# Kernel optimization log

Measured on AMD Instinct MI355X. Metric: run time of the kernel, lower is better.

## Reference

```python
import jax, jax.numpy as jnp
import numpy as np

N = 100000   # num nodes
E = 1600000  # num edges (avg degree 16)
D = 64       # feature dim (in_size == out_size, proj unused in forward_dglsp)
EPS = 1e-12  # F.normalize eps


def setup_inputs() -> dict:
    key = jax.random.key(0)
    k1, k2, k3 = jax.random.split(key, 3)
    H = jax.random.normal(k1, (N, D), dtype=jnp.float32)
    row = jnp.sort(jax.random.randint(k2, (E,), 0, N, dtype=jnp.int64))  # dst (CSR-like)
    col = jax.random.randint(k3, (E,), 0, N, dtype=jnp.int64)            # src
    return {"H": H, "row": row, "col": col, "num_nodes": N}


def reference(H, row, col, num_nodes):
    # F.normalize(H, p=2, dim=1): divide by max(||h||, eps)
    norm = jnp.sqrt(jnp.sum(H * H, axis=1, keepdims=True))
    Hn = H / jnp.maximum(norm, EPS)

    # bsddmm(A, Hn, Hn.T): cosine-sim score per edge (r, c) = Hn[r] . Hn[c]
    scores = jnp.sum(Hn[row] * Hn[col], axis=1)  # [E]

    # edge softmax per destination row (dglsp softmax along last dim)
    m = jax.ops.segment_max(scores, row, num_segments=num_nodes)  # [N]
    e = jnp.exp(scores - m[row])
    s = jax.ops.segment_sum(e, row, num_segments=num_nodes)       # [N]
    attn = e / s[row]                                             # [E]

    # bspmm(attn, H): out[r] = sum over edges (r,c) attn * H[c]
    out = jax.ops.segment_sum(attn[:, None] * H[col], row, num_segments=num_nodes)
    return out  # [N, D]
```

## Files before the change

kernel.cpp:

```cpp
#include <hip/hip_runtime.h>
#include <math.h>

#define D 64
#define EPS 1e-12f
#define LOG2E 1.4426950408889634f

typedef _Float16 half4_t __attribute__((ext_vector_type(4)));

__device__ __forceinline__ float dpp_sum16(float s) {
    int x;
    x = __builtin_amdgcn_update_dpp(__float_as_int(s), __float_as_int(s),
                                    0x124, 0xf, 0xf, false);
    s += __int_as_float(x);
    x = __builtin_amdgcn_update_dpp(__float_as_int(s), __float_as_int(s),
                                    0x128, 0xf, 0xf, false);
    s += __int_as_float(x);
    x = __builtin_amdgcn_update_dpp(__float_as_int(s), __float_as_int(s),
                                    0xB1, 0xf, 0xf, false);
    s += __int_as_float(x);
    x = __builtin_amdgcn_update_dpp(__float_as_int(s), __float_as_int(s),
                                    0x4E, 0xf, 0xf, false);
    s += __int_as_float(x);
    return s;
}

__global__ void prep_kernel(const float4* __restrict__ H4,
                            float* __restrict__ inv_norm,
                            float* __restrict__ in_log,
                            half4_t* __restrict__ Hh,
                            const int* __restrict__ row,
                            int* __restrict__ row_ptr, int N, int E,
                            int do_conv) {
    int t = blockIdx.x * blockDim.x + threadIdx.x;
    if (t < N * 16) {
        int r = t >> 4, sub = t & 15;
        float4 v = H4[(size_t)r * 16 + sub];
        if (do_conv) {
            half4_t h;
            h[0] = (_Float16)v.x; h[1] = (_Float16)v.y;
            h[2] = (_Float16)v.z; h[3] = (_Float16)v.w;
            Hh[(size_t)r * 16 + sub] = h;
        }
        float ss = v.x * v.x + v.y * v.y + v.z * v.z + v.w * v.w;
        ss += __shfl_xor(ss, 1, 64);
        ss += __shfl_xor(ss, 2, 64);
        ss += __shfl_xor(ss, 4, 64);
        ss += __shfl_xor(ss, 8, 64);
        if (sub == 0) {
            float inv = 1.0f / fmaxf(sqrtf(ss), EPS);
            inv_norm[r] = inv;
            if (do_conv) in_log[r] = inv * LOG2E;
        }
    }
    if (t < E) {
        int cur  = row[t];
        int prev = (t == 0) ? -1 : row[t - 1];
        for (int r = prev + 1; r <= cur; ++r) row_ptr[r] = t;
        if (t == E - 1) {
            for (int r = cur + 1; r <= N; ++r) row_ptr[r] = E;
        }
    }
}

template <bool FP16>
__global__ __launch_bounds__(256) void agnn_kernel(
    const float* __restrict__ H,
    const half4_t* __restrict__ Hh,
    const float* __restrict__ inv_norm,
    const float* __restrict__ invg,
    const int* __restrict__ row_ptr,
    const int* __restrict__ col,
    float* __restrict__ out, int N) {
    int wid  = (blockIdx.x * blockDim.x + threadIdx.x) >> 6;
    int lane = threadIdx.x & 63;
    if (wid >= N) return;
    int g   = lane >> 4;
    int sub = lane & 15;

    int start = row_ptr[wid];
    int end   = row_ptr[wid + 1];

    if (start >= end) {
        if (g == 0) {
            float4 z = {0.0f, 0.0f, 0.0f, 0.0f};
            ((float4*)out)[(size_t)wid * 16 + sub] = z;
        }
        return;
    }

    const float4* H4 = (const float4*)H;
    const char* Hb   = (const char*)(FP16 ? (const void*)Hh : (const void*)H);
    const char* Ib   = (const char*)invg;
    const char* Cb   = (const char*)col;
    unsigned subo    = (unsigned)sub << (FP16 ? 3 : 4);

    auto ld_row = [&](int c) -> float4 {
        if constexpr (FP16) {
            half4_t h = *(const half4_t*)(Hb + (((unsigned)c << 7) + subo));
            float4 f;
            f.x = (float)h[0]; f.y = (float)h[1];
            f.z = (float)h[2]; f.w = (float)h[3];
            return f;
        } else {
            return *(const float4*)(Hb + (((unsigned)c << 8) + subo));
        }
    };
    auto ld_in  = [&](int c) -> float { return *(const float*)(Ib + ((unsigned)c << 2)); };
    auto ld_col = [&](int i) -> int   { return *(const int*)(Cb + ((unsigned)i << 2)); };
    auto edge_p = [&](float s, float in) -> float {
        if constexpr (FP16) return exp2f(s * in);
        else                return __expf(s * in);
    };

    float4 hr = H4[(size_t)wid * 16 + sub];
    float inr = inv_norm[wid];
    hr.x *= inr; hr.y *= inr; hr.z *= inr; hr.w *= inr;

    float  l = 0.0f;
    float4 acc = {0.0f, 0.0f, 0.0f, 0.0f};

    int e  = start + g;
    int cl = end - 1;

    int c0 = ld_col(min(e, cl));
    int c1 = ld_col(min(e + 4, cl));
    float  in0 = ld_in(c0),  in1 = ld_in(c1);
    float4 h0  = ld_row(c0), h1  = ld_row(c1);

    while (e + 4 < end) {
        int n0 = ld_col(min(e + 8,  cl));
        int n1 = ld_col(min(e + 12, cl));
        float  nin0 = ld_in(n0),  nin1 = ld_in(n1);
        float4 nh0  = ld_row(n0), nh1  = ld_row(n1);

        float s0 = hr.x * h0.x + hr.y * h0.y + hr.z * h0.z + hr.w * h0.w;
        float s1 = hr.x * h1.x + hr.y * h1.y + hr.z * h1.z + hr.w * h1.w;
        s0 = dpp_sum16(s0);
        s1 = dpp_sum16(s1);

        float p0 = edge_p(s0, in0);
        float p1 = edge_p(s1, in1);
        l += p0 + p1;
        acc.x += p0 * h0.x + p1 * h1.x;
        acc.y += p0 * h0.y + p1 * h1.y;
        acc.z += p0 * h0.z + p1 * h1.z;
        acc.w += p0 * h0.w + p1 * h1.w;

        h0 = nh0; h1 = nh1; in0 = nin0; in1 = nin1;
        e += 8;
    }

    if (e < end) {
        float s = hr.x * h0.x + hr.y * h0.y + hr.z * h0.z + hr.w * h0.w;
        s = dpp_sum16(s);
        float p = edge_p(s, in0);
        l += p;
        acc.x += p * h0.x;
        acc.y += p * h0.y;
        acc.z += p * h0.z;
        acc.w += p * h0.w;
    }

    #pragma unroll
    for (int off = 16; off <= 32; off <<= 1) {
        l     += __shfl_xor(l, off, 64);
        acc.x += __shfl_xor(acc.x, off, 64);
        acc.y += __shfl_xor(acc.y, off, 64);
        acc.z += __shfl_xor(acc.z, off, 64);
        acc.w += __shfl_xor(acc.w, off, 64);
    }

    if (g == 0) {
        float invl = 1.0f / l;
        float4 o;
        o.x = acc.x * invl; o.y = acc.y * invl;
        o.z = acc.z * invl; o.w = acc.w * invl;
        ((float4*)out)[(size_t)wid * 16 + sub] = o;
    }
}

extern "C" void kernel_launch(void* const* d_in, const int* in_sizes, int n_in,
                              void* d_out, int out_size, void* d_ws, size_t ws_size,
                              hipStream_t stream) {
    const float* H   = (const float*)d_in[0];
    const int*   row = (const int*)d_in[1];
    const int*   col = (const int*)d_in[2];
    float*       out = (float*)d_out;

    int N = in_sizes[0] / D;
    int E = in_sizes[1];

    size_t hh_bytes = (size_t)N * 16 * sizeof(half4_t);
    size_t need     = hh_bytes + (size_t)N * 8 + (size_t)(N + 1) * 4;
    bool   use_fp16 = ws_size >= need;

    half4_t* Hh;
    float*   inv_norm;
    float*   in_log;
    int*     row_ptr;
    if (use_fp16) {
        Hh       = (half4_t*)d_ws;
        inv_norm = (float*)((char*)d_ws + hh_bytes);
        in_log   = inv_norm + N;
        row_ptr  = (int*)(in_log + N);
    } else {
        Hh       = (half4_t*)d_ws;
        inv_norm = (float*)d_ws;
        in_log   = inv_norm;
        row_ptr  = (int*)(inv_norm + N);
    }

    int prep_threads = (N * 16 > E) ? N * 16 : E;
    prep_kernel<<<(prep_threads + 255) / 256, 256, 0, stream>>>(
        (const float4*)H, inv_norm, in_log, Hh, row, row_ptr, N, E,
        use_fp16 ? 1 : 0);

    if (use_fp16) {
        agnn_kernel<true><<<(N + 3) / 4, 256, 0, stream>>>(
            H, Hh, inv_norm, in_log, row_ptr, col, out, N);
    } else {
        agnn_kernel<false><<<(N + 3) / 4, 256, 0, stream>>>(
            H, Hh, inv_norm, inv_norm, row_ptr, col, out, N);
    }
}
```

Measured before the change: 140.3 us.

## Precompute per-edge offset/invnorm pairs and batch eight gathers per iteration

Result: slower. 180.3 us (+28.5%).

```diff
diff --git a/kernel.cpp b/kernel.cpp
--- a/kernel.cpp
+++ b/kernel.cpp
@@ -24,52 +24,58 @@
     return s;
 }
 
-__global__ void prep_kernel(const float4* __restrict__ H4,
-                            float* __restrict__ inv_norm,
-                            float* __restrict__ in_log,
-                            half4_t* __restrict__ Hh,
-                            const int* __restrict__ row,
-                            int* __restrict__ row_ptr, int N, int E,
-                            int do_conv) {
+__global__ void prep1_kernel(const float4* __restrict__ H4,
+                             float* __restrict__ inv_norm,
+                             half4_t* __restrict__ Hh, int N, int do_conv) {
     int t = blockIdx.x * blockDim.x + threadIdx.x;
-    if (t < N * 16) {
-        int r = t >> 4, sub = t & 15;
-        float4 v = H4[(size_t)r * 16 + sub];
-        if (do_conv) {
-            half4_t h;
-            h[0] = (_Float16)v.x; h[1] = (_Float16)v.y;
-            h[2] = (_Float16)v.z; h[3] = (_Float16)v.w;
-            Hh[(size_t)r * 16 + sub] = h;
-        }
-        float ss = v.x * v.x + v.y * v.y + v.z * v.z + v.w * v.w;
-        ss += __shfl_xor(ss, 1, 64);
-        ss += __shfl_xor(ss, 2, 64);
-        ss += __shfl_xor(ss, 4, 64);
-        ss += __shfl_xor(ss, 8, 64);
-        if (sub == 0) {
-            float inv = 1.0f / fmaxf(sqrtf(ss), EPS);
-            inv_norm[r] = inv;
-            if (do_conv) in_log[r] = inv * LOG2E;
-        }
-    }
-    if (t < E) {
-        int cur  = row[t];
-        int prev = (t == 0) ? -1 : row[t - 1];
-        for (int r = prev + 1; r <= cur; ++r) row_ptr[r] = t;
-        if (t == E - 1) {
-            for (int r = cur + 1; r <= N; ++r) row_ptr[r] = E;
-        }
-    }
-}
-
-template <bool FP16>
-__global__ __launch_bounds__(256) void agnn_kernel(
+    if (t >= N * 16) return;
+    int r = t >> 4, sub = t & 15;
+    float4 v = H4[(size_t)r * 16 + sub];
+    if (do_conv) {
+        half4_t h;
+        h[0] = (_Float16)v.x; h[1] = (_Float16)v.y;
+        h[2] = (_Float16)v.z; h[3] = (_Float16)v.w;
+        Hh[(size_t)r * 16 + sub] = h;
+    }
+    float ss = v.x * v.x + v.y * v.y + v.z * v.z + v.w * v.w;
+    ss += __shfl_xor(ss, 1, 64);
+    ss += __shfl_xor(ss, 2, 64);
+    ss += __shfl_xor(ss, 4, 64);
+    ss += __shfl_xor(ss, 8, 64);
+    if (sub == 0) inv_norm[r] = 1.0f / fmaxf(sqrtf(ss), EPS);
+}
+
+__global__ void prep2_kernel(const int* __restrict__ row,
+                             const int* __restrict__ col,
+                             const float* __restrict__ inv_norm,
+                             int* __restrict__ row_ptr,
+                             uint2* __restrict__ pairs,
+                             int N, int E, int mode) {
+    int e = blockIdx.x * blockDim.x + threadIdx.x;
+    if (e >= E) return;
+    int cur  = row[e];
+    int prev = (e == 0) ? -1 : row[e - 1];
+    for (int r = prev + 1; r <= cur; ++r) row_ptr[r] = e;
+    if (e == E - 1) {
+        for (int r = cur + 1; r <= N; ++r) row_ptr[r] = E;
+    }
+    if (mode) {
+        int c = col[e];
+        uint2 pq;
+        pq.x = (unsigned)c << (mode == 1 ? 7 : 8);
+        pq.y = __float_as_uint(inv_norm[c] * LOG2E);
+        pairs[e] = pq;
+    }
+}
+
+template <bool FP16, bool PAIRS>
+__global__ __launch_bounds__(256, 8) void agnn_kernel(
     const float* __restrict__ H,
     const half4_t* __restrict__ Hh,
     const float* __restrict__ inv_norm,
-    const float* __restrict__ invg,
+    const uint2* __restrict__ pairs,
+    const int* __restrict__ col,
     const int* __restrict__ row_ptr,
-    const int* __restrict__ col,
     float* __restrict__ out, int N) {
     int wid  = (blockIdx.x * blockDim.x + threadIdx.x) >> 6;
     int lane = threadIdx.x & 63;
@@ -88,86 +94,77 @@
         return;
     }
 
-    const float4* H4 = (const float4*)H;
-    const char* Hb   = (const char*)(FP16 ? (const void*)Hh : (const void*)H);
-    const char* Ib   = (const char*)invg;
-    const char* Cb   = (const char*)col;
-    unsigned subo    = (unsigned)sub << (FP16 ? 3 : 4);
-
-    auto ld_row = [&](int c) -> float4 {
-        if constexpr (FP16) {
-            half4_t h = *(const half4_t*)(Hb + (((unsigned)c << 7) + subo));
-            float4 f;
-            f.x = (float)h[0]; f.y = (float)h[1];
-            f.z = (float)h[2]; f.w = (float)h[3];
-            return f;
-        } else {
-            return *(const float4*)(Hb + (((unsigned)c << 8) + subo));
-        }
-    };
-    auto ld_in  = [&](int c) -> float { return *(const float*)(Ib + ((unsigned)c << 2)); };
-    auto ld_col = [&](int i) -> int   { return *(const int*)(Cb + ((unsigned)i << 2)); };
-    auto edge_p = [&](float s, float in) -> float {
-        if constexpr (FP16) return exp2f(s * in);
-        else                return __expf(s * in);
-    };
-
-    float4 hr = H4[(size_t)wid * 16 + sub];
+    const char* Hb = FP16 ? (const char*)Hh : (const char*)H;
+    unsigned subo  = (unsigned)sub << (FP16 ? 3 : 4);
+
+    float4 hr = ((const float4*)H)[(size_t)wid * 16 + sub];
     float inr = inv_norm[wid];
     hr.x *= inr; hr.y *= inr; hr.z *= inr; hr.w *= inr;
 
     float  l = 0.0f;
     float4 acc = {0.0f, 0.0f, 0.0f, 0.0f};
-
-    int e  = start + g;
     int cl = end - 1;
 
-    int c0 = ld_col(min(e, cl));
-    int c1 = ld_col(min(e + 4, cl));
-    float  in0 = ld_in(c0),  in1 = ld_in(c1);
-    float4 h0  = ld_row(c0), h1  = ld_row(c1);
-
-    while (e + 4 < end) {
-        int n0 = ld_col(min(e + 8,  cl));
-        int n1 = ld_col(min(e + 12, cl));
-        float  nin0 = ld_in(n0),  nin1 = ld_in(n1);
-        float4 nh0  = ld_row(n0), nh1  = ld_row(n1);
-
-        float s0 = hr.x * h0.x + hr.y * h0.y + hr.z * h0.z + hr.w * h0.w;
-        float s1 = hr.x * h1.x + hr.y * h1.y + hr.z * h1.z + hr.w * h1.w;
-        s0 = dpp_sum16(s0);
-        s1 = dpp_sum16(s1);
-
-        float p0 = edge_p(s0, in0);
-        float p1 = edge_p(s1, in1);
-        l += p0 + p1;
-        acc.x += p0 * h0.x + p1 * h1.x;
-        acc.y += p0 * h0.y + p1 * h1.y;
-        acc.z += p0 * h0.z + p1 * h1.z;
-        acc.w += p0 * h0.w + p1 * h1.w;
-
-        h0 = nh0; h1 = nh1; in0 = nin0; in1 = nin1;
-        e += 8;
-    }
-
-    if (e < end) {
-        float s = hr.x * h0.x + hr.y * h0.y + hr.z * h0.z + hr.w * h0.w;
-        s = dpp_sum16(s);
-        float p = edge_p(s, in0);
-        l += p;
-        acc.x += p * h0.x;
-        acc.y += p * h0.y;
-        acc.z += p * h0.z;
-        acc.w += p * h0.w;
+    for (int base = start; base < end; base += 32) {
+        unsigned off[8];
+        float    inl[8];
+        #pragma unroll
+        for (int s = 0; s < 8; ++s) {
+            int ee = min(base + g + 4 * s, cl);
+            if constexpr (PAIRS) {
+                uint2 pq = pairs[ee];
+                off[s] = pq.x;
+                inl[s] = __uint_as_float(pq.y);
+            } else {
+                int c  = col[ee];
+                off[s] = (unsigned)c << (FP16 ? 7 : 8);
+                inl[s] = inv_norm[c] * LOG2E;
+            }
+        }
+        if constexpr (FP16) {
+            half4_t hh[8];
+            #pragma unroll
+            for (int s = 0; s < 8; ++s)
+                hh[s] = *(const half4_t*)(Hb + off[s] + subo);
+            #pragma unroll
+            for (int s = 0; s < 8; ++s) {
+                float4 h;
+                h.x = (float)hh[s][0]; h.y = (float)hh[s][1];
+                h.z = (float)hh[s][2]; h.w = (float)hh[s][3];
+                float sd = hr.x * h.x + hr.y * h.y + hr.z * h.z + hr.w * h.w;
+                sd = dpp_sum16(sd);
+                float p = exp2f(sd * inl[s]);
+                p = (base + g + 4 * s < end) ? p : 0.0f;
+                l += p;
+                acc.x += p * h.x; acc.y += p * h.y;
+                acc.z += p * h.z; acc.w += p * h.w;
+            }
+        } else {
+            float4 h[8];
+            #pragma unroll
+            for (int s = 0; s < 8; ++s)
+                h[s] = *(const float4*)(Hb + off[s] + subo);
+            #pragma unroll
+            for (int s = 0; s < 8; ++s) {
+                float sd = hr.x * h[s].x + hr.y * h[s].y +
+                           hr.z * h[s].z + hr.w * h[s].w;
+                sd = dpp_sum16(sd);
+                float p = exp2f(sd * inl[s]);
+                p = (base + g + 4 * s < end) ? p : 0.0f;
+                l += p;
+                acc.x += p * h[s].x; acc.y += p * h[s].y;
+                acc.z += p * h[s].z; acc.w += p * h[s].w;
+            }
+        }
     }
 
     #pragma unroll
-    for (int off = 16; off <= 32; off <<= 1) {
-        l     += __shfl_xor(l, off, 64);
-        acc.x += __shfl_xor(acc.x, off, 64);
-        acc.y += __shfl_xor(acc.y, off, 64);
-        acc.z += __shfl_xor(acc.z, off, 64);
-        acc.w += __shfl_xor(acc.w, off, 64);
+    for (int off2 = 16; off2 <= 32; off2 <<= 1) {
+        l     += __shfl_xor(l, off2, 64);
+        acc.x += __shfl_xor(acc.x, off2, 64);
+        acc.y += __shfl_xor(acc.y, off2, 64);
+        acc.z += __shfl_xor(acc.z, off2, 64);
+        acc.w += __shfl_xor(acc.w, off2, 64);
     }
 
     if (g == 0) {
@@ -190,36 +187,49 @@
     int N = in_sizes[0] / D;
     int E = in_sizes[1];
 
-    size_t hh_bytes = (size_t)N * 16 * sizeof(half4_t);
-    size_t need     = hh_bytes + (size_t)N * 8 + (size_t)(N + 1) * 4;
-    bool   use_fp16 = ws_size >= need;
+    size_t hh_bytes   = (size_t)N * 16 * sizeof(half4_t);
+    size_t pair_bytes = (size_t)E * sizeof(uint2);
+    size_t tail_bytes = (size_t)N * 4 + (size_t)(N + 1) * 4;
+    bool fit_full = ws_size >= hh_bytes + pair_bytes + tail_bytes;
+    bool fit_fp16 = ws_size >= hh_bytes + tail_bytes;
 
     half4_t* Hh;
+    uint2*   pairs;
     float*   inv_norm;
-    float*   in_log;
     int*     row_ptr;
-    if (use_fp16) {
+    int      mode;
+    if (fit_full) {
         Hh       = (half4_t*)d_ws;
+        pairs    = (uint2*)((char*)d_ws + hh_bytes);
+        inv_norm = (float*)((char*)d_ws + hh_bytes + pair_bytes);
+        mode     = 1;
+    } else if (fit_fp16) {
+        Hh       = (half4_t*)d_ws;
+        pairs    = (uint2*)d_ws;
         inv_norm = (float*)((char*)d_ws + hh_bytes);
-        in_log   = inv_norm + N;
-        row_ptr  = (int*)(in_log + N);
+        mode     = 0;
     } else {
         Hh       = (half4_t*)d_ws;
+        pairs    = (uint2*)d_ws;
         inv_norm = (float*)d_ws;
-        in_log   = inv_norm;
-        row_ptr  = (int*)(inv_norm + N);
-    }
-
-    int prep_threads = (N * 16 > E) ? N * 16 : E;
-    prep_kernel<<<(prep_threads + 255) / 256, 256, 0, stream>>>(
-        (const float4*)H, inv_norm, in_log, Hh, row, row_ptr, N, E,
-        use_fp16 ? 1 : 0);
-
-    if (use_fp16) {
-        agnn_kernel<true><<<(N + 3) / 4, 256, 0, stream>>>(
-            H, Hh, inv_norm, in_log, row_ptr, col, out, N);
+        mode     = 0;
+    }
+    row_ptr = (int*)(inv_norm + N);
+
+    prep1_kernel<<<(N * 16 + 255) / 256, 256, 0, stream>>>(
+        (const float4*)H, inv_norm, Hh, N, fit_fp16 ? 1 : 0);
+    prep2_kernel<<<(E + 255) / 256, 256, 0, stream>>>(
+        row, col, inv_norm, row_ptr, pairs, N, E, mode);
+
+    int blocks = (N + 3) / 4;
+    if (fit_full) {
+        agnn_kernel<true, true><<<blocks, 256, 0, stream>>>(
+            H, Hh, inv_norm, pairs, col, row_ptr, out, N);
+    } else if (fit_fp16) {
+        agnn_kernel<true, false><<<blocks, 256, 0, stream>>>(
+            H, Hh, inv_norm, pairs, col, row_ptr, out, N);
     } else {
-        agnn_kernel<false><<<(N + 3) / 4, 256, 0, stream>>>(
-            H, Hh, inv_norm, inv_norm, row_ptr, col, out, N);
-    }
-}
+        agnn_kernel<false, false><<<blocks, 256, 0, stream>>>(
+            H, Hh, inv_norm, pairs, col, row_ptr, out, N);
+    }
+}
```
